# Kernel optimization log

Hardware: AMD Instinct MI355X
Metric: run time of the kernel (lower is better)

## Reference

```python
import jax, jax.numpy as jnp
import numpy as np
import math

B, NQ, NS, K = 4, 4096, 16384, 16
P, IN, D = 3, 128, 256
H = D // 16   # nhead = out_dim // 16 = 16
HD = D // H   # head_dim = 16
RADIUS = 4.0
EPS = 1e-5


def _ln(x, g, b):
    m = jnp.mean(x, -1, keepdims=True)
    v = jnp.mean((x - m) ** 2, -1, keepdims=True)
    return (x - m) / jnp.sqrt(v + EPS) * g + b


def _pos_enc(x, W_pos, b_pos):
    # LearnablePositionalEncoding: cat([x, cos(Linear(2*pi*x))], -1)
    return jnp.concatenate([x, jnp.cos((2.0 * math.pi * x) @ W_pos + b_pos)], axis=-1)


def setup_inputs() -> dict:
    key = jax.random.key(0)
    ks = jax.random.split(key, 24)
    f32 = jnp.float32

    def w(k, shape):
        return jax.random.uniform(k, shape, f32, -1.0, 1.0) / np.float32(np.sqrt(shape[0]))

    inp = {}
    inp['q_pts'] = jax.random.normal(ks[0], (B, NQ, P), f32)
    inp['s_pts'] = jax.random.normal(ks[1], (B, NS, P), f32)
    inp['src_feats'] = jax.random.normal(ks[2], (B, NS, IN), f32)
    inp['query_feats'] = jax.random.normal(ks[3], (B, NQ, IN), f32)
    # shared proj (in_dim != out_dim, skip_dim=None -> skip_proj is the same Linear)
    inp['W_proj'] = w(ks[4], (IN, D)); inp['b_proj'] = jnp.zeros((D,), f32)
    # positional encoding Linear(p_dim, out_dim - p_dim)
    inp['W_pos'] = w(ks[5], (P, D - P)); inp['b_pos'] = jnp.zeros((D - P,), f32)
    # TransformerDecoderLayer (norm_first) params
    inp['ln1_g'] = jnp.ones((D,), f32); inp['ln1_b'] = jnp.zeros((D,), f32)
    inp['sa_Wv'] = w(ks[6], (D, D)); inp['sa_bv'] = jnp.zeros((D,), f32)
    inp['sa_Wo'] = w(ks[7], (D, D)); inp['sa_bo'] = jnp.zeros((D,), f32)
    inp['ln2_g'] = jnp.ones((D,), f32); inp['ln2_b'] = jnp.zeros((D,), f32)
    inp['ca_Wq'] = w(ks[8], (D, D)); inp['ca_bq'] = jnp.zeros((D,), f32)
    inp['ca_Wk'] = w(ks[9], (D, D)); inp['ca_bk'] = jnp.zeros((D,), f32)
    inp['ca_Wv'] = w(ks[10], (D, D)); inp['ca_bv'] = jnp.zeros((D,), f32)
    inp['ca_Wo'] = w(ks[11], (D, D)); inp['ca_bo'] = jnp.zeros((D,), f32)
    inp['ln3_g'] = jnp.ones((D,), f32); inp['ln3_b'] = jnp.zeros((D,), f32)
    inp['W1'] = w(ks[12], (D, D)); inp['b1'] = jnp.zeros((D,), f32)
    inp['W2'] = w(ks[13], (D, D)); inp['b2'] = jnp.zeros((D,), f32)
    inp['neighb_inds'] = jax.random.randint(ks[14], (B, NQ, K), 0, NS)
    return inp


def reference(q_pts, s_pts, src_feats, query_feats, W_proj, b_proj, W_pos, b_pos,
              ln1_g, ln1_b, sa_Wv, sa_bv, sa_Wo, sa_bo, ln2_g, ln2_b,
              ca_Wq, ca_bq, ca_Wk, ca_bk, ca_Wv, ca_bv, ca_Wo, ca_bo,
              ln3_g, ln3_b, W1, b1, W2, b2, neighb_inds):
    # append shadow point at 1e6 with zero feature row
    s_pts_ = jnp.concatenate([s_pts, jnp.full_like(s_pts[:, :1, :], 1e6)], axis=1)   # [B,NS+1,P]
    src_ = jnp.concatenate([src_feats, jnp.zeros_like(src_feats[:, :1, :])], axis=1)  # [B,NS+1,IN]
    src_p = src_ @ W_proj + b_proj            # proj(src_feats)  [B,NS+1,D]
    qf = query_feats @ W_proj + b_proj        # skip_proj == proj (skip_dim=None)
    inds = neighb_inds % (NS + 1)
    flat = inds.reshape(B, -1, 1)             # [B, NQ*K, 1]
    neighbors = jnp.take_along_axis(s_pts_, jnp.broadcast_to(flat, (B, NQ * K, P)), axis=1).reshape(B, NQ, K, P)
    neighb_x = jnp.take_along_axis(src_p, jnp.broadcast_to(flat, (B, NQ * K, D)), axis=1).reshape(B, NQ, K, D)
    neighbors = neighbors - q_pts[:, :, None, :]
    neighb_x = neighb_x + _pos_enc(neighbors / RADIUS, W_pos, b_pos)
    query_x = qf + _pos_enc(jnp.zeros_like(q_pts), W_pos, b_pos)
    mask = jnp.linalg.norm(neighbors, axis=-1) > RADIUS   # [B,NQ,K], True = invalid key

    x = query_x   # [B,NQ,D]: a length-1 target sequence per query point
    # --- self-attention block (seq len 1 -> softmax == 1 -> only V/O projections matter) ---
    h = _ln(x, ln1_g, ln1_b)
    x = x + (h @ sa_Wv + sa_bv) @ sa_Wo + sa_bo
    # --- cross-attention to K gathered neighbors ---
    h = _ln(x, ln2_g, ln2_b)
    q = (h @ ca_Wq + ca_bq).reshape(B, NQ, H, HD)
    kk = (neighb_x @ ca_Wk + ca_bk).reshape(B, NQ, K, H, HD)
    vv = (neighb_x @ ca_Wv + ca_bv).reshape(B, NQ, K, H, HD)
    scores = jnp.einsum('bnhd,bnkhd->bnhk', q, kk) / np.float32(np.sqrt(HD))
    scores = jnp.where(mask[:, :, None, :], jnp.float32(-1e9), scores)
    att = jax.nn.softmax(scores, axis=-1)
    ctx = jnp.einsum('bnhk,bnkhd->bnhd', att, vv).reshape(B, NQ, D)
    x = x + ctx @ ca_Wo + ca_bo
    # --- feed-forward (dim_feedforward == d_model, relu) ---
    h = _ln(x, ln3_g, ln3_b)
    x = x + jax.nn.relu(h @ W1 + b1) @ W2 + b2
    # original zeroes any NaNs (fully-masked rows); shapes chosen so this is a no-op
    return jnp.nan_to_num(x)
```

## Files before the change

kernel.cpp:

```cpp
#include <hip/hip_runtime.h>
#include <hip/hip_bf16.h>
#include <math.h>
#include <stdint.h>

typedef __attribute__((ext_vector_type(8))) short short8;
typedef __attribute__((ext_vector_type(4))) float floatx4;

#define DEVI __device__ __forceinline__

DEVI float b2f(unsigned short u) {
    union { unsigned int i; float f; } v; v.i = ((unsigned int)u) << 16; return v.f;
}
DEVI unsigned short f2b(float f) {
    unsigned int x = __float_as_uint(f);
    unsigned int r = (x + 0x7fffu + ((x >> 16) & 1u)) >> 16;
    return (unsigned short)r;
}

#define GLD16(gp, lp)                                                            \
    __builtin_amdgcn_global_load_lds(                                            \
        (__attribute__((address_space(1))) unsigned int*)(gp),                   \
        (__attribute__((address_space(3))) unsigned int*)(lp), 16, 0, 0)

static constexpr int NQ = 4096, NS = 16384;
static constexpr int NROW_Q = 4 * NQ;
static constexpr int NROW_S = 4 * NS;
static constexpr float INV2PI = 0.15915494309189535f;

__global__ void k_prep(const float* Wproj, const float* saWv, const float* saWo,
                       const float* caWq, const float* caWk, const float* caWv,
                       const float* caWo, const float* W1, const float* W2,
                       const float* b_pos,
                       unsigned short* wTproj, unsigned short* wTsaWv, unsigned short* wTsaWo,
                       unsigned short* wTcaWq, unsigned short* wTkv, unsigned short* wTcaWo,
                       unsigned short* wTW1, unsigned short* wTW2, float* penc0, float* bp2)
{
    int z = blockIdx.z;
    if (z == 9) {
        if (blockIdx.x == 0 && blockIdx.y == 0) {
            int c = threadIdx.y * 16 + threadIdx.x;
            float v = 0.f;
            if (c >= 3) {
                float rev = b_pos[c - 3] * INV2PI;
                bp2[c - 3] = rev;
                rev -= floorf(rev);
                v = __builtin_amdgcn_cosf(rev);
            }
            penc0[c] = v;
        }
        return;
    }
    int n = blockIdx.x * 16 + threadIdx.x;
    int k = blockIdx.y * 16 + threadIdx.y;
    if (z == 4 || z == 5) {
        int tile = (z == 5 ? 16 : 0) + (n >> 4);
        int kt = k >> 5, lg = (k >> 3) & 3, j = k & 7;
        int lane = lg * 16 + (n & 15);
        wTkv[(size_t)(((tile * 8 + kt) * 64 + lane) * 8 + j)] = f2b(caWk == nullptr ? 0.f :
            (z == 4 ? caWk : caWv)[(size_t)k * 256 + n]);
        return;
    }
    const float* src; unsigned short* dst; int K = 256;
    switch (z) {
        case 0: src = Wproj; dst = wTproj; K = 128; break;
        case 1: src = saWv;  dst = wTsaWv; break;
        case 2: src = saWo;  dst = wTsaWo; break;
        case 3: src = caWq;  dst = wTcaWq; break;
        case 6: src = caWo;  dst = wTcaWo; break;
        case 7: src = W1;    dst = wTW1;   break;
        default: src = W2;   dst = wTW2;   break;
    }
    if (k < K) dst[(size_t)n * K + k] = f2b(src[(size_t)k * 256 + n]);
}

__global__ void k_wfuse(const float* Wv, const float* Wo, const float* bv, const float* bo,
                        unsigned short* wTsa, float* bsa)
{
    int k = blockIdx.x, n = threadIdx.x;
    float s = 0.f;
    for (int c = 0; c < 256; ++c) s = fmaf(Wv[k * 256 + c], Wo[c * 256 + n], s);
    wTsa[n * 256 + k] = f2b(s);
    if (k == 0) {
        float s2 = bo[n];
        for (int c = 0; c < 256; ++c) s2 = fmaf(bv[c], Wo[c * 256 + n], s2);
        bsa[n] = s2;
    }
}

__global__ void k_cvt(const float* in, unsigned short* out, int n4)
{
    int i = blockIdx.x * blockDim.x + threadIdx.x;
    int stride = gridDim.x * blockDim.x;
    for (; i < n4; i += stride) {
        float4 v = ((const float4*)in)[i];
        unsigned long long p =
              (unsigned long long)f2b(v.x)
            | ((unsigned long long)f2b(v.y) << 16)
            | ((unsigned long long)f2b(v.z) << 32)
            | ((unsigned long long)f2b(v.w) << 48);
        ((unsigned long long*)out)[i] = p;
    }
}

template<int EPI>
__global__ __launch_bounds__(256, 2)
void k_gemm(const unsigned short* A, const unsigned short* BT, const float* bias,
            const float* extra, void* outp, int M, int N, int K)
{
    __shared__ alignas(16) unsigned short lA[128 * 64];
    __shared__ alignas(16) unsigned short lB[64 * 64];
    const int tid = threadIdx.x;
    const int wave = tid >> 6, lane = tid & 63;
    const int m0 = blockIdx.x * 128, n0 = blockIdx.y * 64;
    const int wm = (wave >> 1) * 64, wn = (wave & 1) * 32;
    floatx4 acc[4][2] = {};

    for (int kt = 0; kt < K; kt += 64) {
        __syncthreads();
        #pragma unroll
        for (int c = 0; c < 4; ++c) {
            int o = (tid + c * 256) * 16;
            int row = o >> 7, inner = o & 127;
            int srk = inner ^ ((row & 7) << 4);
            GLD16((const char*)A + ((size_t)(m0 + row) * K + kt) * 2 + srk, (char*)lA + o);
        }
        #pragma unroll
        for (int c = 0; c < 2; ++c) {
            int o = (tid + c * 256) * 16;
            int row = o >> 7, inner = o & 127;
            int srk = inner ^ ((row & 7) << 4);
            GLD16((const char*)BT + ((size_t)(n0 + row) * K + kt) * 2 + srk, (char*)lB + o);
        }
        __syncthreads();
        #pragma unroll
        for (int kc = 0; kc < 2; ++kc) {
            const int kb = kc * 64 + ((lane >> 4) << 4);
            short8 bf[2];
            #pragma unroll
            for (int nf = 0; nf < 2; ++nf) {
                int nn = wn + nf * 16 + (lane & 15);
                bf[nf] = *(const short8*)((const char*)lB + nn * 128 + (kb ^ ((nn & 7) << 4)));
            }
            #pragma unroll
            for (int mf = 0; mf < 4; ++mf) {
                int rr = wm + mf * 16 + (lane & 15);
                short8 af = *(const short8*)((const char*)lA + rr * 128 + (kb ^ ((rr & 7) << 4)));
                acc[mf][0] = __builtin_amdgcn_mfma_f32_16x16x32_bf16(af, bf[0], acc[mf][0], 0, 0, 0);
                acc[mf][1] = __builtin_amdgcn_mfma_f32_16x16x32_bf16(af, bf[1], acc[mf][1], 0, 0, 0);
            }
        }
    }
    #pragma unroll
    for (int mf = 0; mf < 4; ++mf)
        #pragma unroll
        for (int nf = 0; nf < 2; ++nf)
            #pragma unroll
            for (int r = 0; r < 4; ++r) {
                int row = m0 + wm + mf * 16 + ((lane >> 4) << 2) + r;
                int col = n0 + wn + nf * 16 + (lane & 15);
                float v = acc[mf][nf][r] + bias[col];
                if (EPI == 4) v += extra[(size_t)row * N + col];
                if (EPI == 1) v = fmaxf(v, 0.f);
                if (EPI == 4) {
                    if (isnan(v)) v = 0.f;
                    else if (isinf(v)) v = v > 0.f ? 3.402823466e38f : -3.402823466e38f;
                }
                if (EPI == 0 || EPI == 1)
                    ((unsigned short*)outp)[(size_t)row * N + col] = f2b(v);
                else
                    ((float*)outp)[(size_t)row * N + col] = v;
            }
}

template<int EPI2>
__global__ __launch_bounds__(256, 2)
void k_gemm_ln(const unsigned short* A, const unsigned short* BT, const float* bias,
               const float* extra, const float* lng, const float* lnb,
               float* outf, unsigned short* outb, int M, int K)
{
    __shared__ alignas(16) unsigned short lA[64 * 64];
    __shared__ alignas(16) unsigned short lB[256 * 64];
    const int tid = threadIdx.x, wave = tid >> 6, lane = tid & 63;
    const int l15 = lane & 15, lg = lane >> 4;
    const int m0 = blockIdx.x * 64;
    floatx4 acc[16] = {};

    for (int kt = 0; kt < K; kt += 64) {
        __syncthreads();
        #pragma unroll
        for (int c = 0; c < 2; ++c) {
            int o = (tid + c * 256) * 16;
            int row = o >> 7, inner = o & 127;
            int srk = inner ^ ((row & 7) << 4);
            GLD16((const char*)A + ((size_t)(m0 + row) * K + kt) * 2 + srk, (char*)lA + o);
        }
        #pragma unroll
        for (int c = 0; c < 8; ++c) {
            int o = (tid + c * 256) * 16;
            int row = o >> 7, inner = o & 127;
            int srk = inner ^ ((row & 7) << 4);
            GLD16((const char*)BT + ((size_t)row * K + kt) * 2 + srk, (char*)lB + o);
        }
        __syncthreads();
        #pragma unroll
        for (int kc = 0; kc < 2; ++kc) {
            const int kb = kc * 64 + (lg << 4);
            int rr = wave * 16 + l15;
            short8 af = *(const short8*)((const char*)lA + rr * 128 + (kb ^ ((rr & 7) << 4)));
            #pragma unroll
            for (int nf = 0; nf < 16; ++nf) {
                int nn = nf * 16 + l15;
                short8 bf = *(const short8*)((const char*)lB + nn * 128 + (kb ^ ((nn & 7) << 4)));
                acc[nf] = __builtin_amdgcn_mfma_f32_16x16x32_bf16(af, bf, acc[nf], 0, 0, 0);
            }
        }
    }

    #pragma unroll
    for (int nf = 0; nf < 16; ++nf) {
        int col = nf * 16 + l15;
        float bi = bias[col] + (EPI2 == 0 ? extra[col] : 0.f);
        #pragma unroll
        for (int r = 0; r < 4; ++r) {
            int row = m0 + wave * 16 + lg * 4 + r;
            float v = acc[nf][r] + bi;
            if (EPI2 == 1) v += extra[(size_t)row * 256 + col];
            acc[nf][r] = v;
            outf[(size_t)row * 256 + col] = v;
        }
    }
    float mean[4], inv[4];
    #pragma unroll
    for (int r = 0; r < 4; ++r) {
        float s = 0.f;
        #pragma unroll
        for (int nf = 0; nf < 16; ++nf) s += acc[nf][r];
        #pragma unroll
        for (int t = 1; t <= 8; t <<= 1) s += __shfl_xor(s, t);
        mean[r] = s * (1.f / 256.f);
        float q = 0.f;
        #pragma unroll
        for (int nf = 0; nf < 16; ++nf) { float d = acc[nf][r] - mean[r]; q += d * d; }
        #pragma unroll
        for (int t = 1; t <= 8; t <<= 1) q += __shfl_xor(q, t);
        inv[r] = 1.0f / sqrtf(q * (1.f / 256.f) + 1e-5f);
    }
    #pragma unroll
    for (int nf = 0; nf < 16; ++nf) {
        int col = nf * 16 + l15;
        float g = lng[col], b = lnb[col];
        #pragma unroll
        for (int r = 0; r < 4; ++r) {
            int row = m0 + wave * 16 + lg * 4 + r;
            outb[(size_t)row * 256 + col] = f2b((acc[nf][r] - mean[r]) * inv[r] * g + b);
        }
    }
}

__global__ __launch_bounds__(256, 4)
void k_attn(const unsigned short* srcp, const unsigned short* qb, const int* inds,
            const float* s_pts, const float* q_pts, const float* W_pos, const float* bp2,
            const unsigned short* wTkv, const float* bv, unsigned short* ctx)
{
    __shared__ alignas(16) unsigned short nx[64 * 256];
    __shared__ alignas(16) float att_lds[4 * 16 * 16];
    __shared__ alignas(16) unsigned short qls[4 * 256];
    __shared__ alignas(16) float dist_lds[64];
    const int tid = threadIdx.x, wave = tid >> 6, lane = tid & 63;
    const int qbase = blockIdx.x * 4;
    const int l15 = lane & 15, lg = lane >> 4;

    if (tid < 128)
        *(uint4*)&qls[tid * 8] = *(const uint4*)(qb + (size_t)qbase * 256 + tid * 8);

    float bvv[4];
    #pragma unroll
    for (int nf = 0; nf < 4; ++nf) bvv[nf] = bv[(wave * 4 + nf) * 16 + l15];

    {
        int r = tid >> 2, sub = tid & 3;
        int qi = qbase + (r >> 4);
        int bb = qi >> 12;
        int k = r & 15;
        int raw = inds[((size_t)qi << 4) + k];
        int idx = raw % (NS + 1); if (idx < 0) idx += NS + 1;
        bool shadow = (idx == NS);
        const int c0 = sub * 64;
        const unsigned short* srow = srcp + ((size_t)bb * NS + (shadow ? 0 : idx)) * 256 + c0;
        short8 sv[8];
        #pragma unroll
        for (int j = 0; j < 8; ++j) sv[j] = *(const short8*)(srow + j * 8);

        float px = q_pts[(size_t)qi * 3], py = q_pts[(size_t)qi * 3 + 1], pz = q_pts[(size_t)qi * 3 + 2];
        float sx, sy, sz;
        if (shadow) { sx = sy = sz = 1e6f; }
        else {
            const float* sp = s_pts + ((size_t)bb * NS + idx) * 3;
            sx = sp[0]; sy = sp[1]; sz = sp[2];
        }
        float tx = (sx - px) * 0.25f, ty = (sy - py) * 0.25f, tz = (sz - pz) * 0.25f;
        if (sub == 0) dist_lds[r] = tx * tx + ty * ty + tz * tz;

        #pragma unroll
        for (int cc = 0; cc < 64; cc += 8) {
            short8 vals;
            #pragma unroll
            for (int j = 0; j < 8; ++j) {
                int c = c0 + cc + j;
                float pe;
                if (c == 0) pe = tx;
                else if (c == 1) pe = ty;
                else if (c == 2) pe = tz;
                else {
                    int jj = c - 3;
                    float rev = fmaf(tx, W_pos[jj],
                                fmaf(ty, W_pos[253 + jj],
                                fmaf(tz, W_pos[506 + jj], bp2[jj])));
                    rev -= floorf(rev);
                    pe = __builtin_amdgcn_cosf(rev);
                }
                float sval = shadow ? 0.f : b2f((unsigned short)sv[cc / 8][j]);
                vals[j] = (short)f2b(sval + pe);
            }
            int byte = (c0 + cc) * 2;
            *(short8*)((char*)nx + r * 512 + (byte ^ ((r & 7) << 4))) = vals;
        }
    }
    __syncthreads();

    floatx4 acc[4][4];

    #pragma unroll
    for (int mf = 0; mf < 4; ++mf)
        #pragma unroll
        for (int nf = 0; nf < 4; ++nf) acc[mf][nf] = floatx4{0.f, 0.f, 0.f, 0.f};

    #pragma unroll 2
    for (int kt = 0; kt < 8; ++kt) {
        const int kb = kt * 64 + (lg << 4);
        short8 bfr[4];
        #pragma unroll
        for (int nf = 0; nf < 4; ++nf) {
            int tile = wave * 4 + nf;
            bfr[nf] = *(const short8*)((const char*)wTkv + (size_t)(((tile * 8 + kt) * 64 + lane) << 4));
        }
        #pragma unroll
        for (int mf = 0; mf < 4; ++mf) {
            int rr = mf * 16 + l15;
            short8 af = *(const short8*)((const char*)nx + rr * 512 + (kb ^ ((rr & 7) << 4)));
            #pragma unroll
            for (int nf = 0; nf < 4; ++nf)
                acc[mf][nf] = __builtin_amdgcn_mfma_f32_16x16x32_bf16(af, bfr[nf], acc[mf][nf], 0, 0, 0);
        }
    }

    {
        #pragma unroll
        for (int mf = 0; mf < 4; ++mf) {
            float4 d4 = *(const float4*)&dist_lds[mf * 16 + lg * 4];
            float dd4[4] = {d4.x, d4.y, d4.z, d4.w};
            #pragma unroll
            for (int nf = 0; nf < 4; ++nf) {
                float qvv = b2f(qls[mf * 256 + (wave * 4 + nf) * 16 + l15]);
                float s[4];
                #pragma unroll
                for (int rr = 0; rr < 4; ++rr) s[rr] = acc[mf][nf][rr] * qvv;
                #pragma unroll
                for (int t = 1; t <= 8; t <<= 1)
                    #pragma unroll
                    for (int rr = 0; rr < 4; ++rr) s[rr] += __shfl_xor(s[rr], t);
                #pragma unroll
                for (int rr = 0; rr < 4; ++rr)
                    s[rr] = (dd4[rr] > 1.0f) ? -1e9f : s[rr] * 0.25f;
                float m = fmaxf(fmaxf(s[0], s[1]), fmaxf(s[2], s[3]));
                m = fmaxf(m, __shfl_xor(m, 16));
                m = fmaxf(m, __shfl_xor(m, 32));
                float p[4], su = 0.f;
                #pragma unroll
                for (int rr = 0; rr < 4; ++rr) { p[rr] = __expf(s[rr] - m); su += p[rr]; }
                su += __shfl_xor(su, 16);
                su += __shfl_xor(su, 32);
                float inv = __builtin_amdgcn_rcpf(su);
                if (l15 == 0) {
                    float4 a4 = {p[0] * inv, p[1] * inv, p[2] * inv, p[3] * inv};
                    *(float4*)&att_lds[(mf * 16 + wave * 4 + nf) * 16 + lg * 4] = a4;
                }
            }
        }
    }

    #pragma unroll
    for (int mf = 0; mf < 4; ++mf)
        #pragma unroll
        for (int nf = 0; nf < 4; ++nf) acc[mf][nf] = floatx4{0.f, 0.f, 0.f, 0.f};

    #pragma unroll 2
    for (int kt = 0; kt < 8; ++kt) {
        const int kb = kt * 64 + (lg << 4);
        short8 bfr[4];
        #pragma unroll
        for (int nf = 0; nf < 4; ++nf) {
            int tile = 16 + wave * 4 + nf;
            bfr[nf] = *(const short8*)((const char*)wTkv + (size_t)(((tile * 8 + kt) * 64 + lane) << 4));
        }
        #pragma unroll
        for (int mf = 0; mf < 4; ++mf) {
            int rr = mf * 16 + l15;
            short8 af = *(const short8*)((const char*)nx + rr * 512 + (kb ^ ((rr & 7) << 4)));
            #pragma unroll
            for (int nf = 0; nf < 4; ++nf)
                acc[mf][nf] = __builtin_amdgcn_mfma_f32_16x16x32_bf16(af, bfr[nf], acc[mf][nf], 0, 0, 0);
        }
    }

    {
        #pragma unroll
        for (int mf = 0; mf < 4; ++mf)
            #pragma unroll
            for (int nf = 0; nf < 4; ++nf) {
                float4 a4 = *(const float4*)&att_lds[(mf * 16 + wave * 4 + nf) * 16 + lg * 4];
                float o = a4.x * acc[mf][nf][0];
                o = fmaf(a4.y, acc[mf][nf][1], o);
                o = fmaf(a4.z, acc[mf][nf][2], o);
                o = fmaf(a4.w, acc[mf][nf][3], o);
                o += __shfl_xor(o, 16);
                o += __shfl_xor(o, 32);
                o += bvv[nf];
                if (lane < 16)
                    ctx[(size_t)(qbase + mf) * 256 + (wave * 4 + nf) * 16 + lane] = f2b(o);
            }
    }
}

extern "C" void kernel_launch(void* const* d_in, const int* in_sizes, int n_in,
                              void* d_out, int out_size, void* d_ws, size_t ws_size,
                              hipStream_t stream)
{
    const float* q_pts   = (const float*)d_in[0];
    const float* s_pts   = (const float*)d_in[1];
    const float* src_f   = (const float*)d_in[2];
    const float* query_f = (const float*)d_in[3];
    const float* W_proj  = (const float*)d_in[4];
    const float* b_proj  = (const float*)d_in[5];
    const float* W_pos   = (const float*)d_in[6];
    const float* b_pos   = (const float*)d_in[7];
    const float* ln1_g   = (const float*)d_in[8];
    const float* ln1_b   = (const float*)d_in[9];
    const float* sa_Wv   = (const float*)d_in[10];
    const float* sa_bv   = (const float*)d_in[11];
    const float* sa_Wo   = (const float*)d_in[12];
    const float* sa_bo   = (const float*)d_in[13];
    const float* ln2_g   = (const float*)d_in[14];
    const float* ln2_b   = (const float*)d_in[15];
    const float* ca_Wq   = (const float*)d_in[16];
    const float* ca_bq   = (const float*)d_in[17];
    const float* ca_Wk   = (const float*)d_in[18];
    const float* ca_Wv   = (const float*)d_in[20];
    const float* ca_bv   = (const float*)d_in[21];
    const float* ca_Wo   = (const float*)d_in[22];
    const float* ca_bo   = (const float*)d_in[23];
    const float* ln3_g   = (const float*)d_in[24];
    const float* ln3_b   = (const float*)d_in[25];
    const float* W1      = (const float*)d_in[26];
    const float* b1      = (const float*)d_in[27];
    const float* W2      = (const float*)d_in[28];
    const float* b2      = (const float*)d_in[29];
    const int*   inds    = (const int*)d_in[30];

    char* ws = (char*)d_ws;
    size_t off = 0;
    auto alloc = [&](size_t bytes) { char* p = ws + off; off += (bytes + 1023) & ~(size_t)1023; return p; };

    unsigned short* wTproj = (unsigned short*)alloc(256 * 128 * 2);
    unsigned short* wTsaWv = (unsigned short*)alloc(256 * 256 * 2);
    unsigned short* wTsaWo = (unsigned short*)alloc(256 * 256 * 2);
    unsigned short* wTcaWq = (unsigned short*)alloc(256 * 256 * 2);
    unsigned short* wTkv   = (unsigned short*)alloc(512 * 256 * 2);
    unsigned short* wTcaWo = (unsigned short*)alloc(256 * 256 * 2);
    unsigned short* wTW1   = (unsigned short*)alloc(256 * 256 * 2);
    unsigned short* wTW2   = (unsigned short*)alloc(256 * 256 * 2);
    unsigned short* wTsa   = (unsigned short*)alloc(256 * 256 * 2);
    float*          bsa    = (float*)alloc(256 * 4);
    float*          penc0  = (float*)alloc(256 * 4);
    float*          bp2    = (float*)alloc(256 * 4);
    unsigned short* srcb   = (unsigned short*)alloc((size_t)NROW_S * 128 * 2);
    unsigned short* qfb    = (unsigned short*)alloc((size_t)NROW_Q * 128 * 2);
    unsigned short* srcp   = (unsigned short*)alloc((size_t)NROW_S * 256 * 2);
    float*          qx     = (float*)alloc((size_t)NROW_Q * 256 * 4);
    unsigned short* hbuf   = (unsigned short*)alloc((size_t)NROW_Q * 256 * 2);
    unsigned short* tbuf   = (unsigned short*)alloc((size_t)NROW_Q * 256 * 2);
    float*          xbuf   = (float*)alloc((size_t)NROW_Q * 256 * 4);
    unsigned short* qbuf   = (unsigned short*)alloc((size_t)NROW_Q * 256 * 2);
    unsigned short* ctxbuf = (unsigned short*)alloc((size_t)NROW_Q * 256 * 2);
    float*          x2buf  = (float*)alloc((size_t)NROW_Q * 256 * 4);

    dim3 bl16(16, 16);
    k_prep<<<dim3(16, 16, 10), bl16, 0, stream>>>(
        W_proj, sa_Wv, sa_Wo, ca_Wq, ca_Wk, ca_Wv, ca_Wo, W1, W2, b_pos,
        wTproj, wTsaWv, wTsaWo, wTcaWq, wTkv, wTcaWo, wTW1, wTW2, penc0, bp2);
    k_wfuse<<<256, 256, 0, stream>>>(sa_Wv, sa_Wo, sa_bv, sa_bo, wTsa, bsa);

    k_cvt<<<1024, 256, 0, stream>>>(src_f, srcb, NROW_S * 128 / 4);
    k_cvt<<<1024, 256, 0, stream>>>(query_f, qfb, NROW_Q * 128 / 4);

    k_gemm<0><<<dim3(512, 4), 256, 0, stream>>>(srcb, wTproj, b_proj, nullptr, srcp, NROW_S, 256, 128);
    k_gemm_ln<0><<<256, 256, 0, stream>>>(qfb, wTproj, b_proj, penc0, ln1_g, ln1_b,
                                          qx, hbuf, NROW_Q, 128);

    k_gemm_ln<1><<<256, 256, 0, stream>>>(hbuf, wTsa, bsa, qx, ln2_g, ln2_b,
                                          xbuf, hbuf, NROW_Q, 256);

    k_gemm<0><<<dim3(128, 4), 256, 0, stream>>>(hbuf, wTcaWq, ca_bq, nullptr, qbuf, NROW_Q, 256, 256);
    k_attn<<<4096, 256, 0, stream>>>(srcp, qbuf, inds, s_pts, q_pts, W_pos, bp2, wTkv, ca_bv, ctxbuf);
    k_gemm_ln<1><<<256, 256, 0, stream>>>(ctxbuf, wTcaWo, ca_bo, xbuf, ln3_g, ln3_b,
                                          x2buf, hbuf, NROW_Q, 256);

    k_gemm<1><<<dim3(128, 4), 256, 0, stream>>>(hbuf, wTW1, b1, nullptr, tbuf, NROW_Q, 256, 256);
    k_gemm<4><<<dim3(128, 4), 256, 0, stream>>>(tbuf, wTW2, b2, x2buf, d_out, NROW_Q, 256, 256);

    (void)in_sizes; (void)n_in; (void)out_size; (void)ws_size;
}
```

Before: 345.1 us.

## Fuse query-side GEMM+LN chain and FFN tail into two kernels

```diff
diff --git a/kernel.cpp b/kernel.cpp
--- a/kernel.cpp
+++ b/kernel.cpp
@@ -27,13 +27,14 @@
 static constexpr int NROW_S = 4 * NS;
 static constexpr float INV2PI = 0.15915494309189535f;
 
-__global__ void k_prep(const float* Wproj, const float* saWv, const float* saWo,
-                       const float* caWq, const float* caWk, const float* caWv,
-                       const float* caWo, const float* W1, const float* W2,
-                       const float* b_pos,
-                       unsigned short* wTproj, unsigned short* wTsaWv, unsigned short* wTsaWo,
-                       unsigned short* wTcaWq, unsigned short* wTkv, unsigned short* wTcaWo,
-                       unsigned short* wTW1, unsigned short* wTW2, float* penc0, float* bp2)
+
+__global__ void k_prep(const float* Wproj, const float* caWq, const float* caWk,
+                       const float* caWv, const float* caWo, const float* W1,
+                       const float* W2, const float* b_pos,
+                       unsigned short* wTproj, unsigned short* wTcaWqf,
+                       unsigned short* wTkv, unsigned short* wTcaWo,
+                       unsigned short* wTW1f, unsigned short* wTW2f,
+                       float* penc0, float* bp2)
 {
     int z = blockIdx.z;
     if (z == 9) {
@@ -50,36 +51,31 @@
         }
         return;
     }
+    if (z == 1 || z == 2) return;
     int n = blockIdx.x * 16 + threadIdx.x;
     int k = blockIdx.y * 16 + threadIdx.y;
-    if (z == 4 || z == 5) {
-        int tile = (z == 5 ? 16 : 0) + (n >> 4);
-        int kt = k >> 5, lg = (k >> 3) & 3, j = k & 7;
-        int lane = lg * 16 + (n & 15);
-        wTkv[(size_t)(((tile * 8 + kt) * 64 + lane) * 8 + j)] = f2b(caWk == nullptr ? 0.f :
-            (z == 4 ? caWk : caWv)[(size_t)k * 256 + n]);
-        return;
-    }
-    const float* src; unsigned short* dst; int K = 256;
-    switch (z) {
-        case 0: src = Wproj; dst = wTproj; K = 128; break;
-        case 1: src = saWv;  dst = wTsaWv; break;
-        case 2: src = saWo;  dst = wTsaWo; break;
-        case 3: src = caWq;  dst = wTcaWq; break;
-        case 6: src = caWo;  dst = wTcaWo; break;
-        case 7: src = W1;    dst = wTW1;   break;
-        default: src = W2;   dst = wTW2;   break;
-    }
-    if (k < K) dst[(size_t)n * K + k] = f2b(src[(size_t)k * 256 + n]);
+    if (z == 0) { if (k < 128) wTproj[(size_t)n * 128 + k] = f2b(Wproj[(size_t)k * 256 + n]); return; }
+    if (z == 6) { wTcaWo[(size_t)n * 256 + k] = f2b(caWo[(size_t)k * 256 + n]); return; }
+    const float* src; unsigned short* dst; int tadd = 0;
+    if (z == 3)      { src = caWq; dst = wTcaWqf; }
+    else if (z == 4) { src = caWk; dst = wTkv; }
+    else if (z == 5) { src = caWv; dst = wTkv; tadd = 16; }
+    else if (z == 7) { src = W1;   dst = wTW1f; }
+    else             { src = W2;   dst = wTW2f; }
+    int tile = tadd + (n >> 4);
+    int kt = k >> 5, lgi = (k >> 3) & 3, j = k & 7;
+    dst[(size_t)((tile * 8 + kt) * 64 + lgi * 16 + (n & 15)) * 8 + j] =
+        f2b(src[(size_t)k * 256 + n]);
 }
 
 __global__ void k_wfuse(const float* Wv, const float* Wo, const float* bv, const float* bo,
-                        unsigned short* wTsa, float* bsa)
+                        unsigned short* wsaf, float* bsa)
 {
     int k = blockIdx.x, n = threadIdx.x;
     float s = 0.f;
     for (int c = 0; c < 256; ++c) s = fmaf(Wv[k * 256 + c], Wo[c * 256 + n], s);
-    wTsa[n * 256 + k] = f2b(s);
+    int tile = n >> 4, kt = k >> 5, lgi = (k >> 3) & 3, j = k & 7;
+    wsaf[(size_t)((tile * 8 + kt) * 64 + lgi * 16 + (n & 15)) * 8 + j] = f2b(s);
     if (k == 0) {
         float s2 = bo[n];
         for (int c = 0; c < 256; ++c) s2 = fmaf(bv[c], Wo[c * 256 + n], s2);
@@ -159,100 +155,262 @@
                 int row = m0 + wm + mf * 16 + ((lane >> 4) << 2) + r;
                 int col = n0 + wn + nf * 16 + (lane & 15);
                 float v = acc[mf][nf][r] + bias[col];
-                if (EPI == 4) v += extra[(size_t)row * N + col];
-                if (EPI == 1) v = fmaxf(v, 0.f);
-                if (EPI == 4) {
-                    if (isnan(v)) v = 0.f;
-                    else if (isinf(v)) v = v > 0.f ? 3.402823466e38f : -3.402823466e38f;
-                }
-                if (EPI == 0 || EPI == 1)
-                    ((unsigned short*)outp)[(size_t)row * N + col] = f2b(v);
-                else
-                    ((float*)outp)[(size_t)row * N + col] = v;
-            }
-}
-
-template<int EPI2>
+                ((unsigned short*)outp)[(size_t)row * N + col] = f2b(v);
+            }
+    (void)extra;
+}
+
+#define LNSTATS(A, MEAN, INV)                                                     \
+    do {                                                                          \
+        _Pragma("unroll")                                                         \
+        for (int r = 0; r < 4; ++r) {                                             \
+            float s_ = 0.f;                                                       \
+            _Pragma("unroll")                                                     \
+            for (int nf = 0; nf < 16; ++nf) s_ += A[nf][r];                       \
+            _Pragma("unroll")                                                     \
+            for (int t = 1; t <= 8; t <<= 1) s_ += __shfl_xor(s_, t);             \
+            MEAN[r] = s_ * (1.f / 256.f);                                         \
+            float q_ = 0.f;                                                       \
+            _Pragma("unroll")                                                     \
+            for (int nf = 0; nf < 16; ++nf) {                                     \
+                float d_ = A[nf][r] - MEAN[r]; q_ += d_ * d_;                     \
+            }                                                                     \
+            _Pragma("unroll")                                                     \
+            for (int t = 1; t <= 8; t <<= 1) q_ += __shfl_xor(q_, t);             \
+            INV[r] = 1.0f / sqrtf(q_ * (1.f / 256.f) + 1e-5f);                    \
+        }                                                                         \
+    } while (0)
+
 __global__ __launch_bounds__(256, 2)
-void k_gemm_ln(const unsigned short* A, const unsigned short* BT, const float* bias,
-               const float* extra, const float* lng, const float* lnb,
-               float* outf, unsigned short* outb, int M, int K)
+void k_qchain(const unsigned short* A, const unsigned short* BT,
+              const float* bproj, const float* penc0,
+              const float* ln1g, const float* ln1b,
+              const unsigned short* wsaf, const float* bsa,
+              const float* ln2g, const float* ln2b,
+              const unsigned short* wqf, const float* bq,
+              float* xbuf, unsigned short* qbuf)
 {
     __shared__ alignas(16) unsigned short lA[64 * 64];
-    __shared__ alignas(16) unsigned short lB[256 * 64];
+    __shared__ alignas(16) unsigned short hB[16 * 64 * 20];
     const int tid = threadIdx.x, wave = tid >> 6, lane = tid & 63;
     const int l15 = lane & 15, lg = lane >> 4;
     const int m0 = blockIdx.x * 64;
-    floatx4 acc[16] = {};
-
-    for (int kt = 0; kt < K; kt += 64) {
+    const int hrow = wave * 16;
+
+    floatx4 aq[16] = {};
+    for (int kt0 = 0; kt0 < 128; kt0 += 64) {
         __syncthreads();
         #pragma unroll
         for (int c = 0; c < 2; ++c) {
             int o = (tid + c * 256) * 16;
             int row = o >> 7, inner = o & 127;
             int srk = inner ^ ((row & 7) << 4);
-            GLD16((const char*)A + ((size_t)(m0 + row) * K + kt) * 2 + srk, (char*)lA + o);
+            GLD16((const char*)A + ((size_t)(m0 + row) * 128 + kt0) * 2 + srk, (char*)lA + o);
         }
         #pragma unroll
         for (int c = 0; c < 8; ++c) {
             int o = (tid + c * 256) * 16;
             int row = o >> 7, inner = o & 127;
             int srk = inner ^ ((row & 7) << 4);
-            GLD16((const char*)BT + ((size_t)row * K + kt) * 2 + srk, (char*)lB + o);
+            GLD16((const char*)BT + ((size_t)row * 128 + kt0) * 2 + srk, (char*)hB + o);
         }
         __syncthreads();
         #pragma unroll
         for (int kc = 0; kc < 2; ++kc) {
             const int kb = kc * 64 + (lg << 4);
-            int rr = wave * 16 + l15;
+            int rr = hrow + l15;
             short8 af = *(const short8*)((const char*)lA + rr * 128 + (kb ^ ((rr & 7) << 4)));
             #pragma unroll
             for (int nf = 0; nf < 16; ++nf) {
                 int nn = nf * 16 + l15;
-                short8 bf = *(const short8*)((const char*)lB + nn * 128 + (kb ^ ((nn & 7) << 4)));
-                acc[nf] = __builtin_amdgcn_mfma_f32_16x16x32_bf16(af, bf, acc[nf], 0, 0, 0);
-            }
-        }
-    }
-
+                short8 bf = *(const short8*)((const char*)hB + nn * 128 + (kb ^ ((nn & 7) << 4)));
+                aq[nf] = __builtin_amdgcn_mfma_f32_16x16x32_bf16(af, bf, aq[nf], 0, 0, 0);
+            }
+        }
+    }
+    #pragma unroll
+    for (int nf = 0; nf < 16; ++nf) {
+        float bi = bproj[nf * 16 + l15] + penc0[nf * 16 + l15];
+        #pragma unroll
+        for (int r = 0; r < 4; ++r) aq[nf][r] += bi;
+    }
+    float mean[4], inv[4];
+    LNSTATS(aq, mean, inv);
+    __syncthreads();
     #pragma unroll
     for (int nf = 0; nf < 16; ++nf) {
         int col = nf * 16 + l15;
-        float bi = bias[col] + (EPI2 == 0 ? extra[col] : 0.f);
+        float g = ln1g[col], b = ln1b[col];
+        #pragma unroll
+        for (int r = 0; r < 4; ++r)
+            hB[nf * 1280 + (hrow + lg * 4 + r) * 20 + l15] =
+                f2b((aq[nf][r] - mean[r]) * inv[r] * g + b);
+    }
+    __syncthreads();
+    floatx4 as[16] = {};
+    #pragma unroll
+    for (int kt = 0; kt < 8; ++kt) {
+        short8 af = *(const short8*)((const char*)hB +
+                     ((kt * 2 + (lg >> 1)) * 1280 + (hrow + l15) * 20 + (lg & 1) * 8) * 2);
+        #pragma unroll
+        for (int nf = 0; nf < 16; ++nf) {
+            short8 bf = *(const short8*)((const char*)wsaf + ((size_t)((nf * 8 + kt) * 64 + lane) << 4));
+            as[nf] = __builtin_amdgcn_mfma_f32_16x16x32_bf16(af, bf, as[nf], 0, 0, 0);
+        }
+    }
+    #pragma unroll
+    for (int nf = 0; nf < 16; ++nf) {
+        int col = nf * 16 + l15;
+        float bi = bsa[col];
         #pragma unroll
         for (int r = 0; r < 4; ++r) {
-            int row = m0 + wave * 16 + lg * 4 + r;
-            float v = acc[nf][r] + bi;
-            if (EPI2 == 1) v += extra[(size_t)row * 256 + col];
-            acc[nf][r] = v;
-            outf[(size_t)row * 256 + col] = v;
-        }
+            float v = as[nf][r] + bi + aq[nf][r];
+            as[nf][r] = v;
+            xbuf[(size_t)(m0 + hrow + lg * 4 + r) * 256 + col] = v;
+        }
+    }
+    LNSTATS(as, mean, inv);
+    __syncthreads();
+    #pragma unroll
+    for (int nf = 0; nf < 16; ++nf) {
+        int col = nf * 16 + l15;
+        float g = ln2g[col], b = ln2b[col];
+        #pragma unroll
+        for (int r = 0; r < 4; ++r)
+            hB[nf * 1280 + (hrow + lg * 4 + r) * 20 + l15] =
+                f2b((as[nf][r] - mean[r]) * inv[r] * g + b);
+    }
+    __syncthreads();
+    #pragma unroll
+    for (int nf = 0; nf < 16; ++nf) aq[nf] = floatx4{0.f, 0.f, 0.f, 0.f};
+    #pragma unroll
+    for (int kt = 0; kt < 8; ++kt) {
+        short8 af = *(const short8*)((const char*)hB +
+                     ((kt * 2 + (lg >> 1)) * 1280 + (hrow + l15) * 20 + (lg & 1) * 8) * 2);
+        #pragma unroll
+        for (int nf = 0; nf < 16; ++nf) {
+            short8 bf = *(const short8*)((const char*)wqf + ((size_t)((nf * 8 + kt) * 64 + lane) << 4));
+            aq[nf] = __builtin_amdgcn_mfma_f32_16x16x32_bf16(af, bf, aq[nf], 0, 0, 0);
+        }
+    }
+    #pragma unroll
+    for (int nf = 0; nf < 16; ++nf) {
+        int col = nf * 16 + l15;
+        float bi = bq[col];
+        #pragma unroll
+        for (int r = 0; r < 4; ++r)
+            qbuf[(size_t)(m0 + hrow + lg * 4 + r) * 256 + col] = f2b(aq[nf][r] + bi);
+    }
+}
+
+__global__ __launch_bounds__(256, 2)
+void k_tail(const unsigned short* ctx, const unsigned short* BT,
+            const float* bo, const float* xbuf,
+            const float* ln3g, const float* ln3b,
+            const unsigned short* w1f, const float* b1,
+            const unsigned short* w2f, const float* b2, float* out)
+{
+    __shared__ alignas(16) unsigned short lA[64 * 64];
+    __shared__ alignas(16) unsigned short hB[16 * 64 * 20];
+    const int tid = threadIdx.x, wave = tid >> 6, lane = tid & 63;
+    const int l15 = lane & 15, lg = lane >> 4;
+    const int m0 = blockIdx.x * 64;
+    const int hrow = wave * 16;
+
+    floatx4 ax[16] = {};
+    for (int kt0 = 0; kt0 < 256; kt0 += 64) {
+        __syncthreads();
+        #pragma unroll
+        for (int c = 0; c < 2; ++c) {
+            int o = (tid + c * 256) * 16;
+            int row = o >> 7, inner = o & 127;
+            int srk = inner ^ ((row & 7) << 4);
+            GLD16((const char*)ctx + ((size_t)(m0 + row) * 256 + kt0) * 2 + srk, (char*)lA + o);
+        }
+        #pragma unroll
+        for (int c = 0; c < 8; ++c) {
+            int o = (tid + c * 256) * 16;
+            int row = o >> 7, inner = o & 127;
+            int srk = inner ^ ((row & 7) << 4);
+            GLD16((const char*)BT + ((size_t)row * 256 + kt0) * 2 + srk, (char*)hB + o);
+        }
+        __syncthreads();
+        #pragma unroll
+        for (int kc = 0; kc < 2; ++kc) {
+            const int kb = kc * 64 + (lg << 4);
+            int rr = hrow + l15;
+            short8 af = *(const short8*)((const char*)lA + rr * 128 + (kb ^ ((rr & 7) << 4)));
+            #pragma unroll
+            for (int nf = 0; nf < 16; ++nf) {
+                int nn = nf * 16 + l15;
+                short8 bf = *(const short8*)((const char*)hB + nn * 128 + (kb ^ ((nn & 7) << 4)));
+                ax[nf] = __builtin_amdgcn_mfma_f32_16x16x32_bf16(af, bf, ax[nf], 0, 0, 0);
+            }
+        }
+    }
+    #pragma unroll
+    for (int nf = 0; nf < 16; ++nf) {
+        int col = nf * 16 + l15;
+        float bi = bo[col];
+        #pragma unroll
+        for (int r = 0; r < 4; ++r)
+            ax[nf][r] += bi + xbuf[(size_t)(m0 + hrow + lg * 4 + r) * 256 + col];
     }
     float mean[4], inv[4];
-    #pragma unroll
-    for (int r = 0; r < 4; ++r) {
-        float s = 0.f;
-        #pragma unroll
-        for (int nf = 0; nf < 16; ++nf) s += acc[nf][r];
-        #pragma unroll
-        for (int t = 1; t <= 8; t <<= 1) s += __shfl_xor(s, t);
-        mean[r] = s * (1.f / 256.f);
-        float q = 0.f;
-        #pragma unroll
-        for (int nf = 0; nf < 16; ++nf) { float d = acc[nf][r] - mean[r]; q += d * d; }
-        #pragma unroll
-        for (int t = 1; t <= 8; t <<= 1) q += __shfl_xor(q, t);
-        inv[r] = 1.0f / sqrtf(q * (1.f / 256.f) + 1e-5f);
-    }
+    LNSTATS(ax, mean, inv);
+    __syncthreads();
     #pragma unroll
     for (int nf = 0; nf < 16; ++nf) {
         int col = nf * 16 + l15;
-        float g = lng[col], b = lnb[col];
+        float g = ln3g[col], b = ln3b[col];
+        #pragma unroll
+        for (int r = 0; r < 4; ++r)
+            hB[nf * 1280 + (hrow + lg * 4 + r) * 20 + l15] =
+                f2b((ax[nf][r] - mean[r]) * inv[r] * g + b);
+    }
+    __syncthreads();
+    floatx4 a1[16] = {};
+    #pragma unroll
+    for (int kt = 0; kt < 8; ++kt) {
+        short8 af = *(const short8*)((const char*)hB +
+                     ((kt * 2 + (lg >> 1)) * 1280 + (hrow + l15) * 20 + (lg & 1) * 8) * 2);
+        #pragma unroll
+        for (int nf = 0; nf < 16; ++nf) {
+            short8 bf = *(const short8*)((const char*)w1f + ((size_t)((nf * 8 + kt) * 64 + lane) << 4));
+            a1[nf] = __builtin_amdgcn_mfma_f32_16x16x32_bf16(af, bf, a1[nf], 0, 0, 0);
+        }
+    }
+    __syncthreads();
+    #pragma unroll
+    for (int nf = 0; nf < 16; ++nf) {
+        float bi = b1[nf * 16 + l15];
+        #pragma unroll
+        for (int r = 0; r < 4; ++r)
+            hB[nf * 1280 + (hrow + lg * 4 + r) * 20 + l15] = f2b(fmaxf(a1[nf][r] + bi, 0.f));
+    }
+    __syncthreads();
+    #pragma unroll
+    for (int nf = 0; nf < 16; ++nf) a1[nf] = floatx4{0.f, 0.f, 0.f, 0.f};
+    #pragma unroll
+    for (int kt = 0; kt < 8; ++kt) {
+        short8 af = *(const short8*)((const char*)hB +
+                     ((kt * 2 + (lg >> 1)) * 1280 + (hrow + l15) * 20 + (lg & 1) * 8) * 2);
+        #pragma unroll
+        for (int nf = 0; nf < 16; ++nf) {
+            short8 bf = *(const short8*)((const char*)w2f + ((size_t)((nf * 8 + kt) * 64 + lane) << 4));
+            a1[nf] = __builtin_amdgcn_mfma_f32_16x16x32_bf16(af, bf, a1[nf], 0, 0, 0);
+        }
+    }
+    #pragma unroll
+    for (int nf = 0; nf < 16; ++nf) {
+        int col = nf * 16 + l15;
+        float bi = b2[col];
         #pragma unroll
         for (int r = 0; r < 4; ++r) {
-            int row = m0 + wave * 16 + lg * 4 + r;
-            outb[(size_t)row * 256 + col] = f2b((acc[nf][r] - mean[r]) * inv[r] * g + b);
+            float v = a1[nf][r] + bi + ax[nf][r];
+            if (isnan(v)) v = 0.f;
+            else if (isinf(v)) v = v > 0.f ? 3.402823466e38f : -3.402823466e38f;
+            out[(size_t)(m0 + hrow + lg * 4 + r) * 256 + col] = v;
         }
     }
 }
@@ -380,9 +538,9 @@
                 for (int rr = 0; rr < 4; ++rr) { p[rr] = __expf(s[rr] - m); su += p[rr]; }
                 su += __shfl_xor(su, 16);
                 su += __shfl_xor(su, 32);
-                float inv = __builtin_amdgcn_rcpf(su);
+                float iv = __builtin_amdgcn_rcpf(su);
                 if (l15 == 0) {
-                    float4 a4 = {p[0] * inv, p[1] * inv, p[2] * inv, p[3] * inv};
+                    float4 a4 = {p[0] * iv, p[1] * iv, p[2] * iv, p[3] * iv};
                     *(float4*)&att_lds[(mf * 16 + wave * 4 + nf) * 16 + lg * 4] = a4;
                 }
             }
@@ -471,52 +629,41 @@
     size_t off = 0;
     auto alloc = [&](size_t bytes) { char* p = ws + off; off += (bytes + 1023) & ~(size_t)1023; return p; };
 
-    unsigned short* wTproj = (unsigned short*)alloc(256 * 128 * 2);
-    unsigned short* wTsaWv = (unsigned short*)alloc(256 * 256 * 2);
-    unsigned short* wTsaWo = (unsigned short*)alloc(256 * 256 * 2);
-    unsigned short* wTcaWq = (unsigned short*)alloc(256 * 256 * 2);
-    unsigned short* wTkv   = (unsigned short*)alloc(512 * 256 * 2);
-    unsigned short* wTcaWo = (unsigned short*)alloc(256 * 256 * 2);
-    unsigned short* wTW1   = (unsigned short*)alloc(256 * 256 * 2);
-    unsigned short* wTW2   = (unsigned short*)alloc(256 * 256 * 2);
-    unsigned short* wTsa   = (unsigned short*)alloc(256 * 256 * 2);
-    float*          bsa    = (float*)alloc(256 * 4);
-    float*          penc0  = (float*)alloc(256 * 4);
-    float*          bp2    = (float*)alloc(256 * 4);
-    unsigned short* srcb   = (unsigned short*)alloc((size_t)NROW_S * 128 * 2);
-    unsigned short* qfb    = (unsigned short*)alloc((size_t)NROW_Q * 128 * 2);
-    unsigned short* srcp   = (unsigned short*)alloc((size_t)NROW_S * 256 * 2);
-    float*          qx     = (float*)alloc((size_t)NROW_Q * 256 * 4);
-    unsigned short* hbuf   = (unsigned short*)alloc((size_t)NROW_Q * 256 * 2);
-    unsigned short* tbuf   = (unsigned short*)alloc((size_t)NROW_Q * 256 * 2);
-    float*          xbuf   = (float*)alloc((size_t)NROW_Q * 256 * 4);
-    unsigned short* qbuf   = (unsigned short*)alloc((size_t)NROW_Q * 256 * 2);
-    unsigned short* ctxbuf = (unsigned short*)alloc((size_t)NROW_Q * 256 * 2);
-    float*          x2buf  = (float*)alloc((size_t)NROW_Q * 256 * 4);
+    unsigned short* wTproj  = (unsigned short*)alloc(256 * 128 * 2);
+    unsigned short* wTcaWqf = (unsigned short*)alloc(256 * 256 * 2);
+    unsigned short* wTkv    = (unsigned short*)alloc(512 * 256 * 2);
+    unsigned short* wTcaWo  = (unsigned short*)alloc(256 * 256 * 2);
+    unsigned short* wTW1f   = (unsigned short*)alloc(256 * 256 * 2);
+    unsigned short* wTW2f   = (unsigned short*)alloc(256 * 256 * 2);
+    unsigned short* wsaf    = (unsigned short*)alloc(256 * 256 * 2);
+    float*          bsa     = (float*)alloc(256 * 4);
+    float*          penc0   = (float*)alloc(256 * 4);
+    float*          bp2     = (float*)alloc(256 * 4);
+    unsigned short* srcb    = (unsigned short*)alloc((size_t)NROW_S * 128 * 2);
+    unsigned short* qfb     = (unsigned short*)alloc((size_t)NROW_Q * 128 * 2);
+    unsigned short* srcp    = (unsigned short*)alloc((size_t)NROW_S * 256 * 2);
+    float*          xbuf    = (float*)alloc((size_t)NROW_Q * 256 * 4);
+    unsigned short* qbuf    = (unsigned short*)alloc((size_t)NROW_Q * 256 * 2);
+    unsigned short* ctxbuf  = (unsigned short*)alloc((size_t)NROW_Q * 256 * 2);
 
     dim3 bl16(16, 16);
     k_prep<<<dim3(16, 16, 10), bl16, 0, stream>>>(
-        W_proj, sa_Wv, sa_Wo, ca_Wq, ca_Wk, ca_Wv, ca_Wo, W1, W2, b_pos,
-        wTproj, wTsaWv, wTsaWo, wTcaWq, wTkv, wTcaWo, wTW1, wTW2, penc0, bp2);
-    k_wfuse<<<256, 256, 0, stream>>>(sa_Wv, sa_Wo, sa_bv, sa_bo, wTsa, bsa);
+        W_proj, ca_Wq, ca_Wk, ca_Wv, ca_Wo, W1, W2, b_pos,
+        wTproj, wTcaWqf, wTkv, wTcaWo, wTW1f, wTW2f, penc0, bp2);
+    k_wfuse<<<256, 256, 0, stream>>>(sa_Wv, sa_Wo, sa_bv, sa_bo, wsaf, bsa);
 
     k_cvt<<<1024, 256, 0, stream>>>(src_f, srcb, NROW_S * 128 / 4);
     k_cvt<<<1024, 256, 0, stream>>>(query_f, qfb, NROW_Q * 128 / 4);
 
     k_gemm<0><<<dim3(512, 4), 256, 0, stream>>>(srcb, wTproj, b_proj, nullptr, srcp, NROW_S, 256, 128);
-    k_gemm_ln<0><<<256, 256, 0, stream>>>(qfb, wTproj, b_proj, penc0, ln1_g, ln1_b,
-                                          qx, hbuf, NROW_Q, 128);
-
-    k_gemm_ln<1><<<256, 256, 0, stream>>>(hbuf, wTsa, bsa, qx, ln2_g, ln2_b,
-                                          xbuf, hbuf, NROW_Q, 256);
-
-    k_gemm<0><<<dim3(128, 4), 256, 0, stream>>>(hbuf, wTcaWq, ca_bq, nullptr, qbuf, NROW_Q, 256, 256);
+
+    k_qchain<<<256, 256, 0, stream>>>(qfb, wTproj, b_proj, penc0, ln1_g, ln1_b,
+                                      wsaf, bsa, ln2_g, ln2_b, wTcaWqf, ca_bq, xbuf, qbuf);
+
     k_attn<<<4096, 256, 0, stream>>>(srcp, qbuf, inds, s_pts, q_pts, W_pos, bp2, wTkv, ca_bv, ctxbuf);
-    k_gemm_ln<1><<<256, 256, 0, stream>>>(ctxbuf, wTcaWo, ca_bo, xbuf, ln3_g, ln3_b,
-                                          x2buf, hbuf, NROW_Q, 256);
-
-    k_gemm<1><<<dim3(128, 4), 256, 0, stream>>>(hbuf, wTW1, b1, nullptr, tbuf, NROW_Q, 256, 256);
-    k_gemm<4><<<dim3(128, 4), 256, 0, stream>>>(tbuf, wTW2, b2, x2buf, d_out, NROW_Q, 256, 256);
+
+    k_tail<<<256, 256, 0, stream>>>(ctxbuf, wTcaWo, ca_bo, xbuf, ln3_g, ln3_b,
+                                    wTW1f, b1, wTW2f, b2, (float*)d_out);
 
     (void)in_sizes; (void)n_in; (void)out_size; (void)ws_size;
 }
```

Measured after the change: 435.8 us. 26.3% more time.
